# Performance work log

Measured on AMD Instinct MI355X. Metric: run time of the kernel, lower is better.

## Reference

```python
import jax, jax.numpy as jnp
import numpy as np

NODE_DIM = 64
OUT_DIM = 64
EDGE_DIM = 64
N_NODES = 50000
N_EDGES = 800000
BN_EPS = 1e-5


def _batchnorm(x, gamma, beta):
    # training-mode BatchNorm1d: biased batch statistics
    mean = jnp.mean(x, axis=0)
    var = jnp.mean((x - mean) ** 2, axis=0)
    return (x - mean) * jax.lax.rsqrt(var + BN_EPS) * gamma + beta


def setup_inputs() -> dict:
    key = jax.random.key(0)
    ks = jax.random.split(key, 16)
    s = 0.05  # weight init scale
    inp = {
        "em": jax.random.normal(ks[0], (N_NODES, NODE_DIM), jnp.float32),
        "edge_index": jax.random.randint(ks[1], (2, N_EDGES), 0, N_NODES, jnp.int64),
        "edge_features": jax.random.normal(ks[2], (N_EDGES, EDGE_DIM), jnp.float32),
        # GINEConv edge linear (edge_dim -> node_dim)
        "W_le": jax.random.normal(ks[3], (EDGE_DIM, NODE_DIM), jnp.float32) * s,
        "b_le": jnp.zeros((NODE_DIM,), jnp.float32),
        # GINEConv nn: Linear(node_dim, out) -> ReLU -> Linear(out, out)
        "W1": jax.random.normal(ks[4], (NODE_DIM, OUT_DIM), jnp.float32) * s,
        "b1": jnp.zeros((OUT_DIM,), jnp.float32),
        "W2": jax.random.normal(ks[5], (OUT_DIM, OUT_DIM), jnp.float32) * s,
        "b2": jnp.zeros((OUT_DIM,), jnp.float32),
        # x BatchNorm affine
        "gx": jnp.ones((OUT_DIM,), jnp.float32),
        "bx": jnp.zeros((OUT_DIM,), jnp.float32),
        # edge MLP: (edge_dim + 2*out) -> out -> out -> out
        "We1": jax.random.normal(ks[6], (EDGE_DIM + 2 * OUT_DIM, OUT_DIM), jnp.float32) * s,
        "be1": jnp.zeros((OUT_DIM,), jnp.float32),
        "We2": jax.random.normal(ks[7], (OUT_DIM, OUT_DIM), jnp.float32) * s,
        "be2": jnp.zeros((OUT_DIM,), jnp.float32),
        "We3": jax.random.normal(ks[8], (OUT_DIM, OUT_DIM), jnp.float32) * s,
        "be3": jnp.zeros((OUT_DIM,), jnp.float32),
        # edge BatchNorm affine
        "ge": jnp.ones((OUT_DIM,), jnp.float32),
        "be": jnp.zeros((OUT_DIM,), jnp.float32),
    }
    return inp


def reference(em, edge_index, edge_features, W_le, b_le, W1, b1, W2, b2, gx, bx,
              We1, be1, We2, be2, We3, be3, ge, be):
    src, dst = edge_index[0], edge_index[1]
    # GINEConv: msg = relu(x_j + lin(edge_attr)), sum-aggregated at target
    msg = jax.nn.relu(em[src] + edge_features @ W_le + b_le)  # [E, node_dim]
    aggr = jax.ops.segment_sum(msg, dst, num_segments=em.shape[0])  # [N, node_dim]
    h = em + aggr  # eps = 0
    h = jax.nn.relu(h @ W1 + b1) @ W2 + b2  # [N, out]
    x_em = jax.nn.relu(_batchnorm(h, gx, bx))
    # edge update: concat(x_em[src], x_em[dst], edge_features)
    edge_mess = jnp.concatenate([x_em[src], x_em[dst], edge_features], axis=1)
    e = jax.nn.relu(edge_mess @ We1 + be1)
    e = jax.nn.relu(e @ We2 + be2)
    e = e @ We3 + be3
    edge_out = jax.nn.relu(_batchnorm(e, ge, be))
    return x_em, edge_out
```

## Files before the change

kernel.cpp:

```cpp
#include <hip/hip_runtime.h>
#include <cstddef>
#include <cstdint>

#define NN 50000
#define NE 800000

typedef __bf16 bf16x8 __attribute__((ext_vector_type(8)));
typedef float  f32x4  __attribute__((ext_vector_type(4)));

__device__ __forceinline__ bf16x8 ldfrag(const __bf16* __restrict__ wfr, int f, int lane) {
    return *reinterpret_cast<const bf16x8*>(wfr + (size_t)(f * 64 + lane) * 8);
}
__device__ __forceinline__ f32x4 mfma16(bf16x8 a, bf16x8 b, f32x4 c) {
    return __builtin_amdgcn_mfma_f32_16x16x32_bf16(a, b, c, 0, 0, 0);
}
__device__ __forceinline__ bool idx_is64(const int* eidx) {
    return ((eidx[1] | eidx[3] | eidx[5] | eidx[7]) == 0);
}
__device__ __forceinline__ int ld_src(const int* eidx, bool is64, int e) {
    return is64 ? eidx[(size_t)2 * e] : eidx[e];
}
__device__ __forceinline__ int ld_dst(const int* eidx, bool is64, int e) {
    return is64 ? eidx[2 * ((size_t)NE + e)] : eidx[(size_t)NE + e];
}
__device__ __forceinline__ bf16x8 cvt8(const float* __restrict__ p) {
    float4 v0 = *reinterpret_cast<const float4*>(p);
    float4 v1 = *reinterpret_cast<const float4*>(p + 4);
    bf16x8 r;
    r[0] = (__bf16)v0.x; r[1] = (__bf16)v0.y; r[2] = (__bf16)v0.z; r[3] = (__bf16)v0.w;
    r[4] = (__bf16)v1.x; r[5] = (__bf16)v1.y; r[6] = (__bf16)v1.z; r[7] = (__bf16)v1.w;
    return r;
}

__global__ __launch_bounds__(256) void prep(const float* __restrict__ wle, const float* __restrict__ w1,
                                            const float* __restrict__ w2, const float* __restrict__ we1,
                                            const float* __restrict__ we2, const float* __restrict__ we3,
                                            __bf16* __restrict__ wfr) {
    int sid = blockIdx.x * 256 + threadIdx.x;
    int f = sid >> 6, lane = sid & 63;
    const float* W; int fo;
    if (f < 8)       { W = wle; fo = 0; }
    else if (f < 16) { W = w1;  fo = 8; }
    else if (f < 24) { W = w2;  fo = 16; }
    else if (f < 48) { W = we1; fo = 24; }
    else if (f < 56) { W = we2; fo = 48; }
    else             { W = we3; fo = 56; }
    int lf = f - fo, kt = lf >> 2, nt = lf & 3;
    int g = lane >> 4, c = lane & 15;
#pragma unroll
    for (int b = 0; b < 8; b++) {
        int k = kt * 32 + g * 8 + b;
        int n = nt * 16 + c;
        wfr[(size_t)(f * 64 + lane) * 8 + b] = (__bf16)W[(size_t)k * 64 + n];
    }
}

__global__ __launch_bounds__(256) void k1(const float* __restrict__ em, const int* __restrict__ eidx,
                                          const float* __restrict__ ef, const __bf16* __restrict__ wfr,
                                          const float* __restrict__ ble, float* __restrict__ nodebuf) {
    __shared__ __bf16 Ash[64][72];
    const int t = threadIdx.x;
    const int base = blockIdx.x * 64;
    {
        const int r = t >> 2, seg = t & 3;
        const float4* p = reinterpret_cast<const float4*>(ef + (size_t)(base + r) * 64 + seg * 16);
#pragma unroll
        for (int i = 0; i < 4; i++) {
            float4 v = p[i];
            int cb = seg * 16 + i * 4;
            Ash[r][cb + 0] = (__bf16)v.x; Ash[r][cb + 1] = (__bf16)v.y;
            Ash[r][cb + 2] = (__bf16)v.z; Ash[r][cb + 3] = (__bf16)v.w;
        }
    }
    const bool is64 = idx_is64(eidx);
    __syncthreads();
    const int lane = t & 63, w = t >> 6, c = lane & 15, g = lane >> 4;
    const int arow = w * 16 + c;
    f32x4 acc[4] = {{0.f,0.f,0.f,0.f},{0.f,0.f,0.f,0.f},{0.f,0.f,0.f,0.f},{0.f,0.f,0.f,0.f}};
#pragma unroll
    for (int kt = 0; kt < 2; kt++) {
        bf16x8 a = *reinterpret_cast<const bf16x8*>(&Ash[arow][kt * 32 + g * 8]);
#pragma unroll
        for (int nt = 0; nt < 4; nt++) acc[nt] = mfma16(a, ldfrag(wfr, kt * 4 + nt, lane), acc[nt]);
    }
#pragma unroll
    for (int rr = 0; rr < 4; rr++) {
        int e = base + w * 16 + g * 4 + rr;
        int sn = ld_src(eidx, is64, e);
        int dn = ld_dst(eidx, is64, e);
#pragma unroll
        for (int nt = 0; nt < 4; nt++) {
            int col = nt * 16 + c;
            float v = acc[nt][rr] + ble[col] + em[(size_t)sn * 64 + col];
            if (v > 0.f) atomicAdd(&nodebuf[(size_t)dn * 64 + col], v);
        }
    }
}

__global__ __launch_bounds__(256) void k2(const float* __restrict__ em, float* __restrict__ nb,
                                          const __bf16* __restrict__ wfr, const float* __restrict__ b1,
                                          const float* __restrict__ b2, float* __restrict__ sums) {
    __shared__ __bf16 Ysh[64][72];
    __shared__ float bs[128];
    const int t = threadIdx.x;
    const int base = blockIdx.x * 64;
    if (t < 128) bs[t] = 0.f;
    __syncthreads();
    const int lane = t & 63, w = t >> 6, c = lane & 15, g = lane >> 4;
    const int arow = base + w * 16 + c;
    const size_t rl = (size_t)(arow < NN ? arow : NN - 1) * 64;
    bf16x8 a[2];
#pragma unroll
    for (int kt = 0; kt < 2; kt++) {
        int off = kt * 32 + g * 8;
        float4 e0 = *reinterpret_cast<const float4*>(em + rl + off);
        float4 e1 = *reinterpret_cast<const float4*>(em + rl + off + 4);
        float4 n0 = *reinterpret_cast<const float4*>(nb + rl + off);
        float4 n1 = *reinterpret_cast<const float4*>(nb + rl + off + 4);
        bf16x8 r;
        r[0] = (__bf16)(e0.x + n0.x); r[1] = (__bf16)(e0.y + n0.y);
        r[2] = (__bf16)(e0.z + n0.z); r[3] = (__bf16)(e0.w + n0.w);
        r[4] = (__bf16)(e1.x + n1.x); r[5] = (__bf16)(e1.y + n1.y);
        r[6] = (__bf16)(e1.z + n1.z); r[7] = (__bf16)(e1.w + n1.w);
        a[kt] = r;
    }
    f32x4 a1[4] = {{0.f,0.f,0.f,0.f},{0.f,0.f,0.f,0.f},{0.f,0.f,0.f,0.f},{0.f,0.f,0.f,0.f}};
#pragma unroll
    for (int kt = 0; kt < 2; kt++)
#pragma unroll
        for (int nt = 0; nt < 4; nt++) a1[nt] = mfma16(a[kt], ldfrag(wfr, 8 + kt * 4 + nt, lane), a1[nt]);
#pragma unroll
    for (int nt = 0; nt < 4; nt++) {
        float bb = b1[nt * 16 + c];
#pragma unroll
        for (int rr = 0; rr < 4; rr++) {
            float v = a1[nt][rr] + bb;
            v = v > 0.f ? v : 0.f;
            Ysh[w * 16 + g * 4 + rr][nt * 16 + c] = (__bf16)v;
        }
    }
    bf16x8 ya[2];
#pragma unroll
    for (int kt = 0; kt < 2; kt++)
        ya[kt] = *reinterpret_cast<const bf16x8*>(&Ysh[w * 16 + c][kt * 32 + g * 8]);
    f32x4 a2[4] = {{0.f,0.f,0.f,0.f},{0.f,0.f,0.f,0.f},{0.f,0.f,0.f,0.f},{0.f,0.f,0.f,0.f}};
#pragma unroll
    for (int kt = 0; kt < 2; kt++)
#pragma unroll
        for (int nt = 0; nt < 4; nt++) a2[nt] = mfma16(ya[kt], ldfrag(wfr, 16 + kt * 4 + nt, lane), a2[nt]);
#pragma unroll
    for (int nt = 0; nt < 4; nt++) {
        int col = nt * 16 + c;
        float bb = b2[col];
        float ss = 0.f, qq = 0.f;
#pragma unroll
        for (int rr = 0; rr < 4; rr++) {
            int row = base + w * 16 + g * 4 + rr;
            if (row < NN) {
                float v = a2[nt][rr] + bb;
                nb[(size_t)row * 64 + col] = v;
                ss += v; qq += v * v;
            }
        }
        ss += __shfl_xor(ss, 16); ss += __shfl_xor(ss, 32);
        qq += __shfl_xor(qq, 16); qq += __shfl_xor(qq, 32);
        if (g == 0) { atomicAdd(&bs[col], ss); atomicAdd(&bs[64 + col], qq); }
    }
    __syncthreads();
    if (t < 128) atomicAdd(&sums[t], bs[t]);
}

__global__ __launch_bounds__(256) void k3(float* __restrict__ nb, const float* __restrict__ sums,
                                          const float* __restrict__ gx, const float* __restrict__ bx,
                                          __bf16* __restrict__ wsx) {
    size_t i4 = (size_t)(blockIdx.x * 256 + threadIdx.x) * 4;
    int col0 = (int)(i4 & 63);
    float4 v = *reinterpret_cast<const float4*>(nb + i4);
    const float* pv = reinterpret_cast<const float*>(&v);
    float o[4]; short so[4];
#pragma unroll
    for (int j = 0; j < 4; j++) {
        int col = col0 + j;
        float m   = sums[col] * (1.0f / 50000.0f);
        float var = sums[64 + col] * (1.0f / 50000.0f) - m * m;
        float inv = rsqrtf(var + 1e-5f);
        float x = (pv[j] - m) * inv * gx[col] + bx[col];
        x = x > 0.f ? x : 0.f;
        o[j] = x;
        so[j] = __builtin_bit_cast(short, (__bf16)x);
    }
    *reinterpret_cast<float4*>(nb + i4) = make_float4(o[0], o[1], o[2], o[3]);
    *reinterpret_cast<short4*>(wsx + i4) = make_short4(so[0], so[1], so[2], so[3]);
}

__global__ __launch_bounds__(256) void k4(const int* __restrict__ eidx, const float* __restrict__ ef,
                                          const __bf16* __restrict__ wsx, const __bf16* __restrict__ wfr,
                                          const float* __restrict__ be1, const float* __restrict__ be2,
                                          const float* __restrict__ be3, float* __restrict__ eout,
                                          float* __restrict__ pws) {
    __shared__ __bf16 Ysh[2][64][72];
    __shared__ float bs[128];
    const int t = threadIdx.x;
    const int blockb = blockIdx.x * 128;
    if (t < 128) bs[t] = 0.f;
    __syncthreads();
    const int lane = t & 63, w = t >> 6, c = lane & 15, g = lane >> 4;
    const bool is64 = idx_is64(eidx);

    int erow[2], sn[2], dn[2];
    bf16x8 xs[2][2], xd[2][2], ea[2][2];
#pragma unroll
    for (int tt = 0; tt < 2; tt++) {
        erow[tt] = blockb + tt * 64 + w * 16 + c;
        sn[tt] = ld_src(eidx, is64, erow[tt]);
        dn[tt] = ld_dst(eidx, is64, erow[tt]);
#pragma unroll
        for (int kt = 0; kt < 2; kt++) {
            int off = kt * 32 + g * 8;
            xs[tt][kt] = *reinterpret_cast<const bf16x8*>(wsx + (size_t)sn[tt] * 64 + off);
            xd[tt][kt] = *reinterpret_cast<const bf16x8*>(wsx + (size_t)dn[tt] * 64 + off);
            ea[tt][kt] = cvt8(ef + (size_t)erow[tt] * 64 + off);
        }
    }
    f32x4 a1[2][4];
#pragma unroll
    for (int tt = 0; tt < 2; tt++)
#pragma unroll
        for (int nt = 0; nt < 4; nt++) a1[tt][nt] = f32x4{0.f,0.f,0.f,0.f};
#pragma unroll
    for (int tt = 0; tt < 2; tt++)
#pragma unroll
        for (int kt = 0; kt < 2; kt++)
#pragma unroll
            for (int nt = 0; nt < 4; nt++) a1[tt][nt] = mfma16(xs[tt][kt], ldfrag(wfr, 24 + kt * 4 + nt, lane), a1[tt][nt]);
#pragma unroll
    for (int tt = 0; tt < 2; tt++)
#pragma unroll
        for (int kt = 0; kt < 2; kt++)
#pragma unroll
            for (int nt = 0; nt < 4; nt++) a1[tt][nt] = mfma16(xd[tt][kt], ldfrag(wfr, 32 + kt * 4 + nt, lane), a1[tt][nt]);
#pragma unroll
    for (int tt = 0; tt < 2; tt++)
#pragma unroll
        for (int kt = 0; kt < 2; kt++)
#pragma unroll
            for (int nt = 0; nt < 4; nt++) a1[tt][nt] = mfma16(ea[tt][kt], ldfrag(wfr, 40 + kt * 4 + nt, lane), a1[tt][nt]);
#pragma unroll
    for (int tt = 0; tt < 2; tt++)
#pragma unroll
        for (int nt = 0; nt < 4; nt++) {
            float bb = be1[nt * 16 + c];
#pragma unroll
            for (int rr = 0; rr < 4; rr++) {
                float v = a1[tt][nt][rr] + bb;
                v = v > 0.f ? v : 0.f;
                Ysh[tt][w * 16 + g * 4 + rr][nt * 16 + c] = (__bf16)v;
            }
        }
    bf16x8 ya[2][2];
#pragma unroll
    for (int tt = 0; tt < 2; tt++)
#pragma unroll
        for (int kt = 0; kt < 2; kt++)
            ya[tt][kt] = *reinterpret_cast<const bf16x8*>(&Ysh[tt][w * 16 + c][kt * 32 + g * 8]);
    f32x4 a2[2][4];
#pragma unroll
    for (int tt = 0; tt < 2; tt++)
#pragma unroll
        for (int nt = 0; nt < 4; nt++) a2[tt][nt] = f32x4{0.f,0.f,0.f,0.f};
#pragma unroll
    for (int tt = 0; tt < 2; tt++)
#pragma unroll
        for (int kt = 0; kt < 2; kt++)
#pragma unroll
            for (int nt = 0; nt < 4; nt++) a2[tt][nt] = mfma16(ya[tt][kt], ldfrag(wfr, 48 + kt * 4 + nt, lane), a2[tt][nt]);
#pragma unroll
    for (int tt = 0; tt < 2; tt++)
#pragma unroll
        for (int nt = 0; nt < 4; nt++) {
            float bb = be2[nt * 16 + c];
#pragma unroll
            for (int rr = 0; rr < 4; rr++) {
                float v = a2[tt][nt][rr] + bb;
                v = v > 0.f ? v : 0.f;
                Ysh[tt][w * 16 + g * 4 + rr][nt * 16 + c] = (__bf16)v;
            }
        }
#pragma unroll
    for (int tt = 0; tt < 2; tt++)
#pragma unroll
        for (int kt = 0; kt < 2; kt++)
            ya[tt][kt] = *reinterpret_cast<const bf16x8*>(&Ysh[tt][w * 16 + c][kt * 32 + g * 8]);
    f32x4 a3[2][4];
#pragma unroll
    for (int tt = 0; tt < 2; tt++)
#pragma unroll
        for (int nt = 0; nt < 4; nt++) a3[tt][nt] = f32x4{0.f,0.f,0.f,0.f};
#pragma unroll
    for (int tt = 0; tt < 2; tt++)
#pragma unroll
        for (int kt = 0; kt < 2; kt++)
#pragma unroll
            for (int nt = 0; nt < 4; nt++) a3[tt][nt] = mfma16(ya[tt][kt], ldfrag(wfr, 56 + kt * 4 + nt, lane), a3[tt][nt]);
#pragma unroll
    for (int tt = 0; tt < 2; tt++)
#pragma unroll
        for (int nt = 0; nt < 4; nt++) {
            int col = nt * 16 + c;
            float bb = be3[col];
            float ss = 0.f, qq = 0.f;
#pragma unroll
            for (int rr = 0; rr < 4; rr++) {
                int e = blockb + tt * 64 + w * 16 + g * 4 + rr;
                float v = a3[tt][nt][rr] + bb;
                eout[(size_t)e * 64 + col] = v;
                ss += v; qq += v * v;
            }
            ss += __shfl_xor(ss, 16); ss += __shfl_xor(ss, 32);
            qq += __shfl_xor(qq, 16); qq += __shfl_xor(qq, 32);
            if (g == 0) { atomicAdd(&bs[col], ss); atomicAdd(&bs[64 + col], qq); }
        }
    __syncthreads();
    if (t < 128) pws[(size_t)t * (NE / 128) + blockIdx.x] = bs[t];
}

__global__ __launch_bounds__(256) void k4r(const float* __restrict__ pws, float* __restrict__ sums) {
    int b = blockIdx.x;
    float s = 0.f;
    for (int i = threadIdx.x; i < NE / 128; i += 256) s += pws[(size_t)b * (NE / 128) + i];
#pragma unroll
    for (int m = 32; m >= 1; m >>= 1) s += __shfl_xor(s, m);
    __shared__ float acc4[4];
    int lane = threadIdx.x & 63, wid = threadIdx.x >> 6;
    if (lane == 0) acc4[wid] = s;
    __syncthreads();
    if (threadIdx.x == 0) sums[128 + b] = acc4[0] + acc4[1] + acc4[2] + acc4[3];
}

__global__ __launch_bounds__(256) void k5(float* __restrict__ eo, const float* __restrict__ sums,
                                          const float* __restrict__ ge, const float* __restrict__ be) {
    size_t i4 = (size_t)(blockIdx.x * 256 + threadIdx.x) * 4;
    int col0 = (int)(i4 & 63);
    float4 v = *reinterpret_cast<const float4*>(eo + i4);
    const float* pv = reinterpret_cast<const float*>(&v);
    float o[4];
#pragma unroll
    for (int j = 0; j < 4; j++) {
        int col = col0 + j;
        float m   = sums[128 + col] * (1.0f / 800000.0f);
        float var = sums[192 + col] * (1.0f / 800000.0f) - m * m;
        float inv = rsqrtf(var + 1e-5f);
        float x = (pv[j] - m) * inv * ge[col] + be[col];
        o[j] = x > 0.f ? x : 0.f;
    }
    *reinterpret_cast<float4*>(eo + i4) = make_float4(o[0], o[1], o[2], o[3]);
}

extern "C" void kernel_launch(void* const* d_in, const int* in_sizes, int n_in,
                              void* d_out, int out_size, void* d_ws, size_t ws_size,
                              hipStream_t stream) {
    const float* em   = (const float*)d_in[0];
    const int*   eidx = (const int*)d_in[1];
    const float* ef   = (const float*)d_in[2];
    const float* b_le = (const float*)d_in[4];
    const float* b1   = (const float*)d_in[6];
    const float* b2   = (const float*)d_in[8];
    const float* gx   = (const float*)d_in[9];
    const float* bx   = (const float*)d_in[10];
    const float* be1  = (const float*)d_in[12];
    const float* be2  = (const float*)d_in[14];
    const float* be3  = (const float*)d_in[16];
    const float* ge   = (const float*)d_in[17];
    const float* be   = (const float*)d_in[18];

    float* out = (float*)d_out;
    float* nodebuf = out;
    float* eout = out + (size_t)NN * 64;

    float*  sums = (float*)d_ws;
    __bf16* wfr  = (__bf16*)((char*)d_ws + 1024);
    __bf16* wsx  = (__bf16*)((char*)d_ws + 1024 + 65536);
    float*  pws  = (float*)((char*)d_ws + 1024 + 65536 + (size_t)NN * 64 * 2);

    hipMemsetAsync(sums, 0, 256 * sizeof(float), stream);
    hipMemsetAsync(nodebuf, 0, (size_t)NN * 64 * sizeof(float), stream);

    prep<<<16, 256, 0, stream>>>((const float*)d_in[3], (const float*)d_in[5], (const float*)d_in[7],
                                 (const float*)d_in[11], (const float*)d_in[13], (const float*)d_in[15], wfr);
    k1<<<NE / 64, 256, 0, stream>>>(em, eidx, ef, wfr, b_le, nodebuf);
    k2<<<(NN + 63) / 64, 256, 0, stream>>>(em, nodebuf, wfr, b1, b2, sums);
    k3<<<(NN * 64) / 1024, 256, 0, stream>>>(nodebuf, sums, gx, bx, wsx);
    k4<<<NE / 128, 256, 0, stream>>>(eidx, ef, wsx, wfr, be1, be2, be3, eout, pws);
    k4r<<<128, 256, 0, stream>>>(pws, sums);
    k5<<<((size_t)NE * 64) / 1024, 256, 0, stream>>>(eout, sums, ge, be);
}
```

Measured before the change: 473.7 us.

## Add nontemporal stores, MFMA priority hints, grid-stride BN kernel, fold memset into prep

Several independent tweaks: prep zeroes the sums buffer, replacing a separate memset launch. The MFMA sections of k4 are bracketed with s_setprio to raise wave priority during matrix math. k4 stores eout with nontemporal stores. k5 precomputes per-column scale and shift into shared memory and becomes a grid-stride loop with 2048 blocks using nontemporal loads and stores. Nontemporal stores in k4 may hurt, since k5 rereads eout right away and the data could otherwise have stayed in cache.

```diff
diff --git a/kernel.cpp b/kernel.cpp
--- a/kernel.cpp
+++ b/kernel.cpp
@@ -35,7 +35,8 @@
 __global__ __launch_bounds__(256) void prep(const float* __restrict__ wle, const float* __restrict__ w1,
                                             const float* __restrict__ w2, const float* __restrict__ we1,
                                             const float* __restrict__ we2, const float* __restrict__ we3,
-                                            __bf16* __restrict__ wfr) {
+                                            __bf16* __restrict__ wfr, float* __restrict__ sums) {
+    if (blockIdx.x == 0) sums[threadIdx.x] = 0.f;
     int sid = blockIdx.x * 256 + threadIdx.x;
     int f = sid >> 6, lane = sid & 63;
     const float* W; int fo;
@@ -227,6 +228,7 @@
     for (int tt = 0; tt < 2; tt++)
 #pragma unroll
         for (int nt = 0; nt < 4; nt++) a1[tt][nt] = f32x4{0.f,0.f,0.f,0.f};
+    __builtin_amdgcn_s_setprio(1);
 #pragma unroll
     for (int tt = 0; tt < 2; tt++)
 #pragma unroll
@@ -245,6 +247,7 @@
         for (int kt = 0; kt < 2; kt++)
 #pragma unroll
             for (int nt = 0; nt < 4; nt++) a1[tt][nt] = mfma16(ea[tt][kt], ldfrag(wfr, 40 + kt * 4 + nt, lane), a1[tt][nt]);
+    __builtin_amdgcn_s_setprio(0);
 #pragma unroll
     for (int tt = 0; tt < 2; tt++)
 #pragma unroll
@@ -268,12 +271,14 @@
     for (int tt = 0; tt < 2; tt++)
 #pragma unroll
         for (int nt = 0; nt < 4; nt++) a2[tt][nt] = f32x4{0.f,0.f,0.f,0.f};
+    __builtin_amdgcn_s_setprio(1);
 #pragma unroll
     for (int tt = 0; tt < 2; tt++)
 #pragma unroll
         for (int kt = 0; kt < 2; kt++)
 #pragma unroll
             for (int nt = 0; nt < 4; nt++) a2[tt][nt] = mfma16(ya[tt][kt], ldfrag(wfr, 48 + kt * 4 + nt, lane), a2[tt][nt]);
+    __builtin_amdgcn_s_setprio(0);
 #pragma unroll
     for (int tt = 0; tt < 2; tt++)
 #pragma unroll
@@ -296,12 +301,14 @@
     for (int tt = 0; tt < 2; tt++)
 #pragma unroll
         for (int nt = 0; nt < 4; nt++) a3[tt][nt] = f32x4{0.f,0.f,0.f,0.f};
+    __builtin_amdgcn_s_setprio(1);
 #pragma unroll
     for (int tt = 0; tt < 2; tt++)
 #pragma unroll
         for (int kt = 0; kt < 2; kt++)
 #pragma unroll
             for (int nt = 0; nt < 4; nt++) a3[tt][nt] = mfma16(ya[tt][kt], ldfrag(wfr, 56 + kt * 4 + nt, lane), a3[tt][nt]);
+    __builtin_amdgcn_s_setprio(0);
 #pragma unroll
     for (int tt = 0; tt < 2; tt++)
 #pragma unroll
@@ -313,7 +320,7 @@
             for (int rr = 0; rr < 4; rr++) {
                 int e = blockb + tt * 64 + w * 16 + g * 4 + rr;
                 float v = a3[tt][nt][rr] + bb;
-                eout[(size_t)e * 64 + col] = v;
+                __builtin_nontemporal_store(v, &eout[(size_t)e * 64 + col]);
                 ss += v; qq += v * v;
             }
             ss += __shfl_xor(ss, 16); ss += __shfl_xor(ss, 32);
@@ -339,21 +346,28 @@
 
 __global__ __launch_bounds__(256) void k5(float* __restrict__ eo, const float* __restrict__ sums,
                                           const float* __restrict__ ge, const float* __restrict__ be) {
-    size_t i4 = (size_t)(blockIdx.x * 256 + threadIdx.x) * 4;
-    int col0 = (int)(i4 & 63);
-    float4 v = *reinterpret_cast<const float4*>(eo + i4);
-    const float* pv = reinterpret_cast<const float*>(&v);
-    float o[4];
-#pragma unroll
-    for (int j = 0; j < 4; j++) {
-        int col = col0 + j;
+    __shared__ float sc[64], sh[64];
+    if (threadIdx.x < 64) {
+        int col = threadIdx.x;
         float m   = sums[128 + col] * (1.0f / 800000.0f);
         float var = sums[192 + col] * (1.0f / 800000.0f) - m * m;
-        float inv = rsqrtf(var + 1e-5f);
-        float x = (pv[j] - m) * inv * ge[col] + be[col];
-        o[j] = x > 0.f ? x : 0.f;
-    }
-    *reinterpret_cast<float4*>(eo + i4) = make_float4(o[0], o[1], o[2], o[3]);
+        float inv = rsqrtf(var + 1e-5f) * ge[col];
+        sc[col] = inv;
+        sh[col] = be[col] - m * inv;
+    }
+    __syncthreads();
+    const size_t total = (size_t)NE * 64 / 4;
+    for (size_t i = (size_t)blockIdx.x * 256 + threadIdx.x; i < total; i += (size_t)gridDim.x * 256) {
+        f32x4 v = __builtin_nontemporal_load(reinterpret_cast<const f32x4*>(eo) + i);
+        int col0 = (int)((i * 4) & 63);
+        f32x4 o;
+#pragma unroll
+        for (int j = 0; j < 4; j++) {
+            float x = v[j] * sc[col0 + j] + sh[col0 + j];
+            o[j] = x > 0.f ? x : 0.f;
+        }
+        __builtin_nontemporal_store(o, reinterpret_cast<f32x4*>(eo) + i);
+    }
 }
 
 extern "C" void kernel_launch(void* const* d_in, const int* in_sizes, int n_in,
@@ -382,15 +396,15 @@
     __bf16* wsx  = (__bf16*)((char*)d_ws + 1024 + 65536);
     float*  pws  = (float*)((char*)d_ws + 1024 + 65536 + (size_t)NN * 64 * 2);
 
-    hipMemsetAsync(sums, 0, 256 * sizeof(float), stream);
     hipMemsetAsync(nodebuf, 0, (size_t)NN * 64 * sizeof(float), stream);
 
     prep<<<16, 256, 0, stream>>>((const float*)d_in[3], (const float*)d_in[5], (const float*)d_in[7],
-                                 (const float*)d_in[11], (const float*)d_in[13], (const float*)d_in[15], wfr);
+                                 (const float*)d_in[11], (const float*)d_in[13], (const float*)d_in[15],
+                                 wfr, sums);
     k1<<<NE / 64, 256, 0, stream>>>(em, eidx, ef, wfr, b_le, nodebuf);
     k2<<<(NN + 63) / 64, 256, 0, stream>>>(em, nodebuf, wfr, b1, b2, sums);
     k3<<<(NN * 64) / 1024, 256, 0, stream>>>(nodebuf, sums, gx, bx, wsx);
     k4<<<NE / 128, 256, 0, stream>>>(eidx, ef, wsx, wfr, be1, be2, be3, eout, pws);
     k4r<<<128, 256, 0, stream>>>(pws, sums);
-    k5<<<((size_t)NE * 64) / 1024, 256, 0, stream>>>(eout, sums, ge, be);
-}
+    k5<<<2048, 256, 0, stream>>>(eout, sums, ge, be);
+}
```

Measured after the change: 443.3 us, median of 3. 6.4% less time.
